# Optimization experiments

Measured on AMD Instinct MI355X. Metric: run time of the kernel, lower is better.

Reference implementation:

```python
import jax, jax.numpy as jnp
import numpy as np


def _mk_mlp(key, cout):
    dims = [3, 16, 32, 64, 128, cout]
    ws, bs = [], []
    for i in range(5):
        key, k = jax.random.split(key)
        ws.append(jax.random.normal(k, (dims[i], dims[i + 1]), jnp.float32) * (1.0 / np.sqrt(dims[i])))
        bs.append(jnp.zeros((dims[i + 1],), jnp.float32))
    return ws, bs


def setup_inputs() -> dict:
    key = jax.random.key(0)
    k1, k2, k3, k4 = jax.random.split(key, 4)
    B, H, W = 2, 359, 639  # direction-feature grid; LR input is (H+1, W+1)
    direction_feature = jax.random.uniform(k1, (B, 3, H, W), jnp.float32)
    LR_input = jax.random.uniform(k2, (B, 3, H + 1, W + 1), jnp.float32)
    w1, b1 = _mk_mlp(k3, 64)   # MLP1: 3->16->32->64->128->64
    w2, b2 = _mk_mlp(k4, 1)    # MLP2: 3->16->32->64->128->1
    inp = {"direction_feature": direction_feature, "LR_input": LR_input}
    for i in range(5):
        inp[f"m1_w{i}"] = w1[i]; inp[f"m1_b{i}"] = b1[i]
        inp[f"m2_w{i}"] = w2[i]; inp[f"m2_b{i}"] = b2[i]
    return inp


def _pixel_mlp(x, ws, bs):
    # x: [P, 3] -> [P, Cout]; tanh between layers, linear last (as in PixelMLP)
    h = x
    for i in range(4):
        h = jnp.tanh(h @ ws[i] + bs[i])
    return h @ ws[4] + bs[4]


def _dist2():
    # Gaussian4x4PerPixel buffer: [4 dirs, 4, 4] squared distances to 4 subpixel centers
    coords = jnp.arange(4, dtype=jnp.float32)
    yy, xx = jnp.meshgrid(coords, coords, indexing='ij')
    centers = jnp.array([[1.25, 1.25], [1.25, 1.75], [1.75, 1.25], [1.75, 1.75]], jnp.float32)
    cy = centers[:, 0][:, None, None]
    cx = centers[:, 1][:, None, None]
    return (yy[None] - cy) ** 2 + (xx[None] - cx) ** 2  # [4,4,4]


def reference(direction_feature, LR_input,
              m1_w0, m1_w1, m1_w2, m1_w3, m1_w4, m1_b0, m1_b1, m1_b2, m1_b3, m1_b4,
              m2_w0, m2_w1, m2_w2, m2_w3, m2_w4, m2_b0, m2_b1, m2_b2, m2_b3, m2_b4):
    w1 = [m1_w0, m1_w1, m1_w2, m1_w3, m1_w4]; b1 = [m1_b0, m1_b1, m1_b2, m1_b3, m1_b4]
    w2 = [m2_w0, m2_w1, m2_w2, m2_w3, m2_w4]; b2 = [m2_b0, m2_b1, m2_b2, m2_b3, m2_b4]
    B, _, H, W = direction_feature.shape
    P = B * H * W
    pix = direction_feature.transpose(0, 2, 3, 1).reshape(P, 3)  # per-pixel features

    # F_r = sigmoid(MLP1(df)) : [P, 64]; s = sigmoid(MLP2(df)) + 0.05 : [P, 1]
    F_r = jax.nn.sigmoid(_pixel_mlp(pix, w1, b1))
    s = jax.nn.sigmoid(_pixel_mlp(pix, w2, b2)) + 0.05

    dist2 = _dist2().reshape(1, 4, 16)                  # [1,4,16]
    g = jnp.exp(-dist2 / (2.0 * s[:, :, None]))          # [P,4,16]
    g = g / (g.sum(-1, keepdims=True) + 1e-12)

    filt = g * F_r.reshape(P, 4, 16)                     # F_s * F_r
    sum16 = filt.sum(-1, keepdims=True) + 1e-12          # [P,4,1]
    filt = filt / sum16
    filters = filt.reshape(B, H, W, 4, 16).transpose(0, 3, 4, 1, 2)  # [B,4,16,H,W]
    sum16_out = sum16.reshape(B, H, W, 4, 1).transpose(0, 3, 4, 1, 2)  # [B,4,1,H,W]

    # unfold(LR_input, k=4, pad=1, stride=1) -> [B,3,16,H,W]  (k index = ky*4+kx)
    xp = jnp.pad(LR_input, ((0, 0), (0, 0), (1, 1), (1, 1)))
    patches = jnp.stack([xp[:, :, i:i + H, j:j + W] for i in range(4) for j in range(4)], axis=2)

    y = jnp.einsum('bckhw,bdkhw->bcdhw', patches, filters)          # [B,3,4,H,W]
    y = y.reshape(B, 3, 2, 2, H, W).transpose(0, 1, 4, 2, 5, 3)      # [B,3,H,2,W,2]
    y_up = y.reshape(B, 3, H * 2, W * 2)
    return y_up, sum16_out
```

## Files before the change

### kernel.cpp

```cpp
#include <hip/hip_runtime.h>

typedef unsigned short u16;
typedef unsigned int u32;
typedef unsigned long long u64;
typedef short short8 __attribute__((ext_vector_type(8)));
typedef float f32x4 __attribute__((ext_vector_type(4)));

#define DEV static __device__ __forceinline__

DEV float ex2(float x){ return __builtin_amdgcn_exp2f(x); }
DEV float rcpf_(float x){ return __builtin_amdgcn_rcpf(x); }
DEV float bf2f(u16 v){ union {u32 u; float f;} c; c.u=((u32)v)<<16; return c.f; }
DEV u16 f2bf(float f){ union {u32 u; float f;} c; c.f=f; u32 r=c.u+0x7fffu+((c.u>>16)&1u); return (u16)(r>>16); }

DEV float tanh_ps(float v){
    float t = ex2(v);
    return 1.f - 2.f*rcpf_(t+1.f);
}
DEV float sigm_ps(float v){
    return rcpf_(1.f + ex2(v));
}
DEV u32 cvtpk(float lo, float hi){
    u32 r;
    asm("v_cvt_pk_bf16_f32 %0, %1, %2" : "=v"(r) : "v"(lo), "v"(hi));
    return r;
}
DEV short8 ld8(const u16* p){
    union { u64 q[2]; short8 v; } u;
    u.q[0] = *(const u64*)(p);
    u.q[1] = *(const u64*)(p+4);
    return u.v;
}
DEV f32x4 mfma16(short8 a, short8 b, f32x4 c){
    return __builtin_amdgcn_mfma_f32_16x16x32_bf16(a, b, c, 0, 0, 0);
}

struct PrepArgs { const float* w[8]; const float* b[8]; const float* l1w[2]; const float* l1b[2]; };

__global__ void prep_kernel(PrepArgs pa, float* ws){
    u16* whi = (u16*)ws;
    float* bo = ws + 16384;
    const int K_[8]  = {16,32,64,128, 16,32,64,128};
    const int N_[8]  = {32,64,128,64, 32,64,128,1};
    const int NT_[8] = {2,4,8,4, 2,4,8,1};
    const int FB_[8] = {0,1024,3072,11264, 19456,20480,22528,30720};
    const int BB_[8] = {0,32,96,224, 288,320,384,512};
    const float CT_ = 2.8853900817779268f;
    const float CS_ = -1.4426950408889634f;
    const float SC_[8] = {CT_,CT_,CT_,CS_, CT_,CT_,CT_,CS_};
    int tid = blockIdx.x*256 + threadIdx.x;
    if (tid < 32768){
        int l = 0;
#pragma unroll
        for (int i=1;i<8;++i) if (tid >= FB_[i]) l = i;
        int idx = tid - FB_[l];
        int ktnt = idx >> 9;
        int nt = ktnt % NT_[l], kt = ktnt / NT_[l];
        int lane = (idx >> 3) & 63;
        int i = idx & 7;
        int k = kt*32 + ((lane>>4)<<3) + i;
        int n = nt*16 + (lane&15);
        const float* wsrc = pa.w[l];
        float v = (k < K_[l] && n < N_[l]) ? SC_[l]*wsrc[k*N_[l] + n] : 0.f;
        whi[tid] = f2bf(v);
    } else if (tid < 32768 + 528){
        int t = tid - 32768;
        int l = 0;
#pragma unroll
        for (int i=1;i<8;++i) if (t >= BB_[i]) l = i;
        int n = t - BB_[l];
        bo[t] = (n < N_[l]) ? SC_[l]*pa.b[l][n] : 0.f;
    } else if (tid < 33296 + 128){
        int t = tid - 33296;
        if (t < 48)       ws[16912+t]     = CT_*pa.l1w[0][t];
        else if (t < 64)  ws[16960+t-48]  = CT_*pa.l1b[0][t-48];
        else if (t < 112) ws[16976+t-64]  = CT_*pa.l1w[1][t-64];
        else              ws[17024+t-112] = CT_*pa.l1b[1][t-112];
    }
}

DEV void l1_valu(float x0,float x1,float x2, const float* w, const float* bias,
                 u16* buf, int lane){
    int pxl = lane & 31, jb = (lane>>5)*8;
    float v[8];
#pragma unroll
    for (int j=0;j<8;++j){
        int jj = jb + j;
        v[j] = tanh_ps(bias[jj] + x0*w[jj] + x1*w[16+jj] + x2*w[32+jj]);
    }
    union { u32 d[2]; u64 q; } q0, q1;
    q0.d[0]=cvtpk(v[0],v[1]); q0.d[1]=cvtpk(v[2],v[3]);
    q1.d[0]=cvtpk(v[4],v[5]); q1.d[1]=cvtpk(v[6],v[7]);
    *(u64*)(buf + pxl*132 + jb)      = q0.q;
    *(u64*)(buf + pxl*132 + jb+4)    = q1.q;
    *(u64*)(buf + pxl*132 + 16+jb)   = 0ull;
    *(u64*)(buf + pxl*132 + 16+jb+4) = 0ull;
}

template<int KT, int CT, int ACT>
DEV void layer(u16* buf, const u16* wf, const float* bias, float* sPre, int lane){
    short8 x[2][KT];
    int col = lane & 15, koff = (lane>>4)<<3;
#pragma unroll
    for (int pt=0;pt<2;++pt)
#pragma unroll
    for (int kt=0;kt<KT;++kt)
        x[pt][kt] = ld8(buf + (pt*16 + col)*132 + kt*32 + koff);
    asm volatile("" ::: "memory");
#pragma unroll 2
    for (int ct=0; ct<CT; ++ct){
        f32x4 acc[2];
        acc[0]=(f32x4){0.f,0.f,0.f,0.f};
        acc[1]=(f32x4){0.f,0.f,0.f,0.f};
#pragma unroll
        for (int kt=0;kt<KT;++kt){
            short8 wv = *(const short8*)(wf + (((kt*CT+ct)<<6) + lane)*8);
#pragma unroll
            for (int pt=0;pt<2;++pt) acc[pt] = mfma16(wv, x[pt][kt], acc[pt]);
        }
        if constexpr (ACT==2){
            float v0 = acc[0][0] + bias[0];
            float v1 = acc[1][0] + bias[0];
            if ((lane>>4)==0){ sPre[col]=v0; sPre[16+col]=v1; }
        } else {
            int chb = ct*16 + ((lane>>4)<<2);
            float4 bv = *(const float4*)(bias + chb);
#pragma unroll
            for (int pt=0;pt<2;++pt){
                float v0 = acc[pt][0] + bv.x;
                float v1 = acc[pt][1] + bv.y;
                float v2 = acc[pt][2] + bv.z;
                float v3 = acc[pt][3] + bv.w;
                if constexpr (ACT==0){
                    v0=tanh_ps(v0); v1=tanh_ps(v1); v2=tanh_ps(v2); v3=tanh_ps(v3);
                } else {
                    v0=sigm_ps(v0); v1=sigm_ps(v1); v2=sigm_ps(v2); v3=sigm_ps(v3);
                }
                union { u32 d[2]; u64 q; } qq;
                qq.d[0]=cvtpk(v0,v1); qq.d[1]=cvtpk(v2,v3);
                *(u64*)(buf + (pt*16 + col)*132 + chb) = qq.q;
            }
        }
    }
}

__global__ __launch_bounds__(64, 4)
void dlut_kernel(const float* __restrict__ df, const float* __restrict__ lr,
                 const float* __restrict__ ws, float* __restrict__ out){
    constexpr int Hh=359, Ww=639, HW=Hh*Ww, NP=2*HW, LHW=360*640;
    __shared__ u16 sX[32][132];
    __shared__ float sPre[32];

    const u16* whi = (const u16*)ws;
    const float* bo = ws + 16384;

    int lane = threadIdx.x;
    int pxl = lane & 31, hv = lane >> 5;
    int p = blockIdx.x * 32 + pxl;

    float x0=0.f, x1=0.f, x2=0.f;
    int b=0, r2=0, hh=0, wwp=0;
    if (p < NP){
        b = p/HW; r2 = p - b*HW; hh = r2/Ww; wwp = r2 - hh*Ww;
        x0 = df[(b*3+0)*HW + r2];
        x1 = df[(b*3+1)*HW + r2];
        x2 = df[(b*3+2)*HW + r2];
    }

    l1_valu(x0,x1,x2, ws+16976, ws+17024, &sX[0][0], lane);
    __syncthreads();
    layer<1,2,0>(&sX[0][0], whi+19456, bo+288, sPre, lane);
    __syncthreads();
    layer<1,4,0>(&sX[0][0], whi+20480, bo+320, sPre, lane);
    __syncthreads();
    layer<2,8,0>(&sX[0][0], whi+22528, bo+384, sPre, lane);
    __syncthreads();
    layer<4,1,2>(&sX[0][0], whi+30720, bo+512, sPre, lane);
    __syncthreads();
    l1_valu(x0,x1,x2, ws+16912, ws+16960, &sX[0][0], lane);
    __syncthreads();
    layer<1,2,0>(&sX[0][0], whi+0,     bo+0,   sPre, lane);
    __syncthreads();
    layer<1,4,0>(&sX[0][0], whi+1024,  bo+32,  sPre, lane);
    __syncthreads();
    layer<2,8,0>(&sX[0][0], whi+3072,  bo+96,  sPre, lane);
    __syncthreads();
    layer<4,4,1>(&sX[0][0], whi+11264, bo+224, sPre, lane);
    __syncthreads();

    if (p < NP){
        float s = sigm_ps(sPre[pxl]) + 0.05f;
        float E1 = ex2(-0.045084220f * rcpf_(s));
        float F2=E1*E1, F4=F2*F2, F8=F4*F4, F16=F8*F8, F32=F16*F16;
        float F9=F8*E1, F25=F16*F9, F49=F32*F16*E1;
        bool hb = (hv!=0);
        float ry[4];
        ry[0]= hb?F49:F25; ry[1]= hb?F9:E1; ry[2]= hb?E1:F9; ry[3]= hb?F25:F49;
        float cx0[4] = {F25,E1,F9,F49};
        float cx1[4] = {F49,F9,E1,F25};

        float pvv[3][16];
#pragma unroll
        for (int ky=0;ky<4;++ky){
            int yy=hh+ky-1;
            int yyc = yy<0?0:(yy>359?359:yy);
            bool oky = (yy>=0)&&(yy<360);
#pragma unroll
            for (int kx=0;kx<4;++kx){
                int xx=wwp+kx-1;
                int xxc = xx<0?0:(xx>639?639:xx);
                bool ok = oky&&(xx>=0)&&(xx<640);
                int k=ky*4+kx;
                int base = (b*3)*LHW + yyc*640 + xxc;
#pragma unroll
                for (int c=0;c<3;++c){
                    float v = lr[base + c*LHW];
                    pvv[c][k] = ok ? v : 0.f;
                }
            }
        }
#pragma unroll
        for (int dd=0; dd<2; ++dd){
            int d = hv*2 + dd;
            float t[16]; float gs=0.f, T=0.f;
#pragma unroll
            for (int k=0;k<16;++k){
                float cxv = (dd==0) ? cx0[k&3] : cx1[k&3];
                float gk = ry[k>>2]*cxv;
                float fr = bf2f(sX[pxl][d*16+k]);
                float tk = gk*fr;
                gs += gk; T += tk;
                t[k] = tk;
            }
            float rg = rcpf_(gs + 1e-12f);
            float s16v = T*rg + 1e-12f;
            float sc2 = rg * rcpf_(s16v);
            float y0=0.f,y1=0.f,y2=0.f;
#pragma unroll
            for (int k=0;k<16;++k){
                y0+=pvv[0][k]*t[k]; y1+=pvv[1][k]*t[k]; y2+=pvv[2][k]*t[k];
            }
            y0*=sc2; y1*=sc2; y2*=sc2;
            int dy=d>>1, dx=d&1;
            int rc = (2*hh+dy)*1278 + 2*wwp+dx;
            out[((b*3+0)*718)*1278 + rc] = y0;
            out[((b*3+1)*718)*1278 + rc] = y1;
            out[((b*3+2)*718)*1278 + rc] = y2;
            out[5505624 + ((b*4+d)*359 + hh)*639 + wwp] = s16v;
        }
    }
}

extern "C" void kernel_launch(void* const* d_in, const int* in_sizes, int n_in,
                              void* d_out, int out_size, void* d_ws, size_t ws_size,
                              hipStream_t stream){
    const float* df=(const float*)d_in[0];
    const float* lr=(const float*)d_in[1];
    PrepArgs pa;
    for (int i=0;i<4;++i){
        pa.w[i]   = (const float*)d_in[2+4*(i+1)];
        pa.b[i]   = (const float*)d_in[3+4*(i+1)];
        pa.w[4+i] = (const float*)d_in[4+4*(i+1)];
        pa.b[4+i] = (const float*)d_in[5+4*(i+1)];
    }
    pa.l1w[0] = (const float*)d_in[2];  pa.l1b[0] = (const float*)d_in[3];
    pa.l1w[1] = (const float*)d_in[4];  pa.l1b[1] = (const float*)d_in[5];

    float* ws = (float*)d_ws;
    hipLaunchKernelGGL(prep_kernel, dim3(131), dim3(256), 0, stream, pa, ws);

    constexpr int NP = 2*359*639;
    hipLaunchKernelGGL(dlut_kernel, dim3((NP+31)/32), dim3(64), 0, stream,
                       df, lr, (const float*)ws, (float*)d_out);
}
```

Baseline: 94.03 us.

## Use two independent waves per block with wave-local LDS sync, bias-initialized MFMA, vector patch loads

Each block now has two 64-lane waves, each with its own LDS buffer. The block-wide barriers between MLP layers become a wave-local LDS wait (s_waitcnt lgkmcnt(0)), which relies on each wave only touching its own buffer. Biases are preloaded and used as the MFMA accumulator's starting value, so the per-output bias adds go away. Interior pixels read their 4x4 LR patch with unaligned float4 loads instead of scalar gathers. The risk is correctness, since cross-lane LDS visibility within a wave now depends on the waitcnt alone.

```diff
diff --git a/kernel.cpp b/kernel.cpp
--- a/kernel.cpp
+++ b/kernel.cpp
@@ -31,9 +31,13 @@
     u.q[1] = *(const u64*)(p+4);
     return u.v;
 }
+DEV float4 ld4u(const float* p){
+    float4 v; __builtin_memcpy(&v, p, 16); return v;
+}
 DEV f32x4 mfma16(short8 a, short8 b, f32x4 c){
     return __builtin_amdgcn_mfma_f32_16x16x32_bf16(a, b, c, 0, 0, 0);
 }
+#define LGKM0() asm volatile("s_waitcnt lgkmcnt(0)" ::: "memory")
 
 struct PrepArgs { const float* w[8]; const float* b[8]; const float* l1w[2]; const float* l1b[2]; };
 
@@ -106,12 +110,22 @@
 #pragma unroll
     for (int kt=0;kt<KT;++kt)
         x[pt][kt] = ld8(buf + (pt*16 + col)*132 + kt*32 + koff);
+    float4 bvs[CT];
+#pragma unroll
+    for (int ct=0;ct<CT;++ct){
+        if constexpr (ACT==2){
+            float b0 = bias[0];
+            bvs[ct] = (float4){b0,b0,b0,b0};
+        } else {
+            bvs[ct] = *(const float4*)(bias + ct*16 + ((lane>>4)<<2));
+        }
+    }
     asm volatile("" ::: "memory");
 #pragma unroll 2
     for (int ct=0; ct<CT; ++ct){
         f32x4 acc[2];
-        acc[0]=(f32x4){0.f,0.f,0.f,0.f};
-        acc[1]=(f32x4){0.f,0.f,0.f,0.f};
+        acc[0]=(f32x4){bvs[ct].x,bvs[ct].y,bvs[ct].z,bvs[ct].w};
+        acc[1]=acc[0];
 #pragma unroll
         for (int kt=0;kt<KT;++kt){
             short8 wv = *(const short8*)(wf + (((kt*CT+ct)<<6) + lane)*8);
@@ -119,18 +133,15 @@
             for (int pt=0;pt<2;++pt) acc[pt] = mfma16(wv, x[pt][kt], acc[pt]);
         }
         if constexpr (ACT==2){
-            float v0 = acc[0][0] + bias[0];
-            float v1 = acc[1][0] + bias[0];
-            if ((lane>>4)==0){ sPre[col]=v0; sPre[16+col]=v1; }
+            if ((lane>>4)==0){ sPre[col]=acc[0][0]; sPre[16+col]=acc[1][0]; }
         } else {
             int chb = ct*16 + ((lane>>4)<<2);
-            float4 bv = *(const float4*)(bias + chb);
 #pragma unroll
             for (int pt=0;pt<2;++pt){
-                float v0 = acc[pt][0] + bv.x;
-                float v1 = acc[pt][1] + bv.y;
-                float v2 = acc[pt][2] + bv.z;
-                float v3 = acc[pt][3] + bv.w;
+                float v0 = acc[pt][0];
+                float v1 = acc[pt][1];
+                float v2 = acc[pt][2];
+                float v3 = acc[pt][3];
                 if constexpr (ACT==0){
                     v0=tanh_ps(v0); v1=tanh_ps(v1); v2=tanh_ps(v2); v3=tanh_ps(v3);
                 } else {
@@ -144,19 +155,23 @@
     }
 }
 
-__global__ __launch_bounds__(64, 4)
+__global__ __launch_bounds__(128, 4)
 void dlut_kernel(const float* __restrict__ df, const float* __restrict__ lr,
                  const float* __restrict__ ws, float* __restrict__ out){
     constexpr int Hh=359, Ww=639, HW=Hh*Ww, NP=2*HW, LHW=360*640;
-    __shared__ u16 sX[32][132];
-    __shared__ float sPre[32];
+    __shared__ u16 sX[2][32][132];
+    __shared__ float sPreA[2][32];
 
     const u16* whi = (const u16*)ws;
     const float* bo = ws + 16384;
 
-    int lane = threadIdx.x;
+    int wv   = threadIdx.x >> 6;
+    int lane = threadIdx.x & 63;
+    u16* buf   = &sX[wv][0][0];
+    float* sPre = &sPreA[wv][0];
+
     int pxl = lane & 31, hv = lane >> 5;
-    int p = blockIdx.x * 32 + pxl;
+    int p = blockIdx.x*64 + wv*32 + pxl;
 
     float x0=0.f, x1=0.f, x2=0.f;
     int b=0, r2=0, hh=0, wwp=0;
@@ -167,26 +182,26 @@
         x2 = df[(b*3+2)*HW + r2];
     }
 
-    l1_valu(x0,x1,x2, ws+16976, ws+17024, &sX[0][0], lane);
-    __syncthreads();
-    layer<1,2,0>(&sX[0][0], whi+19456, bo+288, sPre, lane);
-    __syncthreads();
-    layer<1,4,0>(&sX[0][0], whi+20480, bo+320, sPre, lane);
-    __syncthreads();
-    layer<2,8,0>(&sX[0][0], whi+22528, bo+384, sPre, lane);
-    __syncthreads();
-    layer<4,1,2>(&sX[0][0], whi+30720, bo+512, sPre, lane);
-    __syncthreads();
-    l1_valu(x0,x1,x2, ws+16912, ws+16960, &sX[0][0], lane);
-    __syncthreads();
-    layer<1,2,0>(&sX[0][0], whi+0,     bo+0,   sPre, lane);
-    __syncthreads();
-    layer<1,4,0>(&sX[0][0], whi+1024,  bo+32,  sPre, lane);
-    __syncthreads();
-    layer<2,8,0>(&sX[0][0], whi+3072,  bo+96,  sPre, lane);
-    __syncthreads();
-    layer<4,4,1>(&sX[0][0], whi+11264, bo+224, sPre, lane);
-    __syncthreads();
+    l1_valu(x0,x1,x2, ws+16976, ws+17024, buf, lane);
+    LGKM0();
+    layer<1,2,0>(buf, whi+19456, bo+288, sPre, lane);
+    LGKM0();
+    layer<1,4,0>(buf, whi+20480, bo+320, sPre, lane);
+    LGKM0();
+    layer<2,8,0>(buf, whi+22528, bo+384, sPre, lane);
+    LGKM0();
+    layer<4,1,2>(buf, whi+30720, bo+512, sPre, lane);
+    LGKM0();
+    l1_valu(x0,x1,x2, ws+16912, ws+16960, buf, lane);
+    LGKM0();
+    layer<1,2,0>(buf, whi+0,     bo+0,   sPre, lane);
+    LGKM0();
+    layer<1,4,0>(buf, whi+1024,  bo+32,  sPre, lane);
+    LGKM0();
+    layer<2,8,0>(buf, whi+3072,  bo+96,  sPre, lane);
+    LGKM0();
+    layer<4,4,1>(buf, whi+11264, bo+224, sPre, lane);
+    LGKM0();
 
     if (p < NP){
         float s = sigm_ps(sPre[pxl]) + 0.05f;
@@ -200,22 +215,36 @@
         float cx1[4] = {F49,F9,E1,F25};
 
         float pvv[3][16];
-#pragma unroll
-        for (int ky=0;ky<4;++ky){
-            int yy=hh+ky-1;
-            int yyc = yy<0?0:(yy>359?359:yy);
-            bool oky = (yy>=0)&&(yy<360);
-#pragma unroll
-            for (int kx=0;kx<4;++kx){
-                int xx=wwp+kx-1;
-                int xxc = xx<0?0:(xx>639?639:xx);
-                bool ok = oky&&(xx>=0)&&(xx<640);
-                int k=ky*4+kx;
-                int base = (b*3)*LHW + yyc*640 + xxc;
-#pragma unroll
-                for (int c=0;c<3;++c){
-                    float v = lr[base + c*LHW];
-                    pvv[c][k] = ok ? v : 0.f;
+        bool interior = (hh>=1) & (hh<=357) & (wwp>=1) & (wwp<=637);
+        if (interior){
+            int base0 = (b*3)*LHW + (hh-1)*640 + (wwp-1);
+#pragma unroll
+            for (int c=0;c<3;++c){
+#pragma unroll
+                for (int ky=0;ky<4;++ky){
+                    float4 v = ld4u(lr + base0 + c*LHW + ky*640);
+                    pvv[c][ky*4+0]=v.x; pvv[c][ky*4+1]=v.y;
+                    pvv[c][ky*4+2]=v.z; pvv[c][ky*4+3]=v.w;
+                }
+            }
+        } else {
+#pragma unroll
+            for (int ky=0;ky<4;++ky){
+                int yy=hh+ky-1;
+                int yyc = yy<0?0:(yy>359?359:yy);
+                bool oky = (yy>=0)&&(yy<360);
+#pragma unroll
+                for (int kx=0;kx<4;++kx){
+                    int xx=wwp+kx-1;
+                    int xxc = xx<0?0:(xx>639?639:xx);
+                    bool ok = oky&&(xx>=0)&&(xx<640);
+                    int k=ky*4+kx;
+                    int base = (b*3)*LHW + yyc*640 + xxc;
+#pragma unroll
+                    for (int c=0;c<3;++c){
+                        float v = lr[base + c*LHW];
+                        pvv[c][k] = ok ? v : 0.f;
+                    }
                 }
             }
         }
@@ -227,7 +256,7 @@
             for (int k=0;k<16;++k){
                 float cxv = (dd==0) ? cx0[k&3] : cx1[k&3];
                 float gk = ry[k>>2]*cxv;
-                float fr = bf2f(sX[pxl][d*16+k]);
+                float fr = bf2f(buf[pxl*132 + d*16+k]);
                 float tk = gk*fr;
                 gs += gk; T += tk;
                 t[k] = tk;
@@ -270,6 +299,6 @@
     hipLaunchKernelGGL(prep_kernel, dim3(131), dim3(256), 0, stream, pa, ws);
 
     constexpr int NP = 2*359*639;
-    hipLaunchKernelGGL(dlut_kernel, dim3((NP+31)/32), dim3(64), 0, stream,
+    hipLaunchKernelGGL(dlut_kernel, dim3((NP+63)/64), dim3(128), 0, stream,
                        df, lr, (const float*)ws, (float*)d_out);
 }
```

After: 163.8 us. +74.2%, slower.
